# Kernel tuning notes

Measured on AMD Instinct MI355X. Metric: run time of the kernel, lower is better.

Reference implementation:

```python
import jax, jax.numpy as jnp
import numpy as np

ALPHA = 0.5
REG_RATIO = 0.5


def _xavier(key, shape):
    fan_in, fan_out = shape
    lim = np.sqrt(6.0 / (fan_in + fan_out))
    return jax.random.uniform(key, shape, minval=-lim, maxval=lim, dtype=jnp.float32)


def setup_inputs() -> dict:
    key = jax.random.key(0)
    ks = jax.random.split(key, 5)
    B, T, I, H, O = 128, 512, 4, 512, 3
    return {
        "x": jax.random.normal(ks[0], (B, T, I), dtype=jnp.float32),
        "h": jax.random.normal(ks[1], (B, H), dtype=jnp.float32),
        "W_rec": _xavier(ks[2], (H, H)),
        "W_in": _xavier(ks[3], (I, H)),
        "W_out": _xavier(ks[4], (H, O)),
        "bias_rec": jnp.zeros((H,), dtype=jnp.float32),
        "bias_in": jnp.zeros((H,), dtype=jnp.float32),
    }


def reference(x, h, W_rec, W_in, W_out, bias_rec, bias_in):
    # x: (B, T, I), h: (B, H)
    B, T, _ = x.shape
    H = h.shape[1]
    n_reg = round(H * REG_RATIO)
    alpha = jnp.asarray(ALPHA, x.dtype)
    # add_noise=False -> noise term is zero
    xt = jnp.swapaxes(x, 0, 1)                     # (T, B, I)
    flags = (jnp.arange(T) > 0).astype(x.dtype)    # z_old reg term skipped at t=0

    def step(carry, inp):
        h_prev, z_prev, reg = carry
        x_t, flag = inp
        # z = W_rec-recurrence + input drive (h_rec + h_in in the torch code)
        z_new = jnp.tanh(h_prev) @ W_rec + bias_rec + x_t @ W_in + bias_in  # (B, H)
        h_new = (1.0 - alpha) * h_prev + alpha * z_new
        # note: h_from_prev / (1 - alpha) == h_prev
        reg = (reg
               + jnp.sum((h_new[:, :n_reg] - h_prev[:, :n_reg]) ** 2)
               + flag * jnp.sum((z_new[:, :n_reg] - z_prev[:, :n_reg]) ** 2))
        out = h_new @ W_out                        # (B, O)
        return (h_new, z_new, reg), (h_new, out)

    init = (h, jnp.zeros_like(h), jnp.asarray(0.0, x.dtype))
    (_, _, reg), (hs, outs) = jax.lax.scan(step, init, (xt, flags))

    hidden_states = jnp.concatenate([h[None], hs], axis=0)  # (T+1, B, H)
    outputs = jnp.swapaxes(outs, 0, 1)                      # (B, T, O)
    tcr_reg = reg / T / B / n_reg
    return outputs, hidden_states, tcr_reg
```

## Files before the change

### kernel.cpp

```cpp
#include <hip/hip_runtime.h>
#include <math.h>


#define BB 128
#define TT 512
#define II 4
#define HH 512
#define OO 3
#define NREG_ 256

#define NTHREADS 512
#define MEMBERS 4
#define ROWS 2
#define NGROUPS 64
#define NBLOCKS (NGROUPS * MEMBERS)

typedef unsigned long long u64;
typedef unsigned int u32;
typedef __attribute__((ext_vector_type(2))) float f32x2;

__device__ __forceinline__ u64 aload(const u64* p) {
    return __hip_atomic_load(p, __ATOMIC_RELAXED, __HIP_MEMORY_SCOPE_AGENT);
}
__device__ __forceinline__ void astore(u64* p, u64 v) {
    __hip_atomic_store(p, v, __ATOMIC_RELAXED, __HIP_MEMORY_SCOPE_AGENT);
}
__device__ __forceinline__ float fast_tanh(float x) {
    float ax = fabsf(x);
    float e  = __expf(2.0f * ax);
    float r  = 1.0f - 2.0f * __builtin_amdgcn_rcpf(e + 1.0f);
    return copysignf(r, x);
}

#define R16(M) M(0) M(1) M(2) M(3) M(4) M(5) M(6) M(7) \
               M(8) M(9) M(10) M(11) M(12) M(13) M(14) M(15)

#define WLD(Q) \
    f32x2 w##Q##a, w##Q##b, w##Q##c, w##Q##d; \
    w##Q##a.x = Wp[(size_t)(4*Q+0)*HH]; w##Q##a.y = Wp[(size_t)(4*Q+0)*HH+64]; \
    w##Q##b.x = Wp[(size_t)(4*Q+1)*HH]; w##Q##b.y = Wp[(size_t)(4*Q+1)*HH+64]; \
    w##Q##c.x = Wp[(size_t)(4*Q+2)*HH]; w##Q##c.y = Wp[(size_t)(4*Q+2)*HH+64]; \
    w##Q##d.x = Wp[(size_t)(4*Q+3)*HH]; w##Q##d.y = Wp[(size_t)(4*Q+3)*HH+64];

#define KSTEP(K, W) { \
    u32 a0_ = __builtin_amdgcn_readlane(__float_as_uint(ar0), (K)); \
    u32 a1_ = __builtin_amdgcn_readlane(__float_as_uint(ar1), (K)); \
    u64 ab_ = (u64)a0_ | ((u64)a1_ << 32); \
    asm("v_pk_fma_f32 %0, %2, %3, %0 op_sel_hi:[1,0,1]\n\t" \
        "v_pk_fma_f32 %1, %2, %3, %1 op_sel:[0,1,0] op_sel_hi:[1,1,1]" \
        : "+v"(accA), "+v"(accB) : "s"(ab_), "v"(W)); }

#define MV(Q) KSTEP(4*Q+0, w##Q##a) KSTEP(4*Q+1, w##Q##b) \
              KSTEP(4*Q+2, w##Q##c) KSTEP(4*Q+3, w##Q##d)

__global__ __launch_bounds__(NTHREADS) __attribute__((amdgpu_waves_per_eu(2, 2)))
void rnn_main(const float* __restrict__ x,
              const float* __restrict__ h0,
              const float* __restrict__ W_rec,
              const float* __restrict__ W_in,
              const float* __restrict__ bias_rec,
              const float* __restrict__ bias_in,
              float* __restrict__ hidden,
              u64* __restrict__ abuf,
              float* __restrict__ partials)
{
    const int tid  = threadIdx.x;
    const int bid  = blockIdx.x;
    const int xcd  = bid & 7;
    const int onx  = bid >> 3;
    const int memb = onx & (MEMBERS - 1);
    const int group = xcd * 8 + (onx >> 2);
    const int r0   = group * ROWS;
    const int wid  = tid >> 6;
    const int lane = tid & 63;

    __shared__ float sc_s[2][ROWS][128][9];
    __shared__ float xbuf[ROWS * TT * II];
    __shared__ float win_s[II][128];
    __shared__ float ub_s[128];
    __shared__ float red_s[NTHREADS / 64];

    for (int idx = tid; idx < ROWS * TT * II; idx += NTHREADS) {
        int r = idx >> 11, rem = idx & (TT * II - 1);
        xbuf[idx] = x[(size_t)(r0 + r) * (TT * II) + rem];
    }
    if (tid < II * 128) {
        int i = tid >> 7, jj = tid & 127;
        win_s[i][jj] = W_in[i * HH + memb * 128 + jj];
    }
    if (tid < 128) {
        ub_s[tid] = bias_rec[memb * 128 + tid] + bias_in[memb * 128 + tid];
    }

    const float* Wp = W_rec + (size_t)(wid * 64) * HH + memb * 128 + lane;
    R16(WLD)

    const int fr  = tid >> 7;
    const int fj  = tid & 127;
    const int fjg = memb * 128 + fj;
    float hprev = 0.0f, zprev = 0.0f, racc = 0.0f;
    if (tid < ROWS * 128) {
        hprev = h0[(size_t)(r0 + fr) * HH + fjg];
        float a0v = fast_tanh(hprev);
        u64 pv = (u64)__float_as_uint(a0v) | ((u64)1u << 32);
        astore(&abuf[((size_t)(0 * BB + r0 + fr)) * HH + fjg], pv);
        hidden[(size_t)(r0 + fr) * HH + fjg] = hprev;
    }

#pragma unroll 1
    for (int t = 0; t < TT; ++t) {
        const int slot = t & 1;
        const u32 tagc = (u32)(t + 1);
        const u32 tagp = (u32)(t + 2);

        const u64* p0 = abuf + ((size_t)(slot * BB + r0)) * HH + wid * 64 + lane;
        const u64* p1 = p0 + HH;
        u64 u0, u1;
        for (;;) {
            u0 = aload(p0);
            u1 = aload(p1);
            bool ok = ((u32)(u0 >> 32) == tagc) & ((u32)(u1 >> 32) == tagc);
            if (__all(ok)) break;
        }
        float ar0 = __uint_as_float((u32)u0);
        float ar1 = __uint_as_float((u32)u1);

        f32x2 accA = {0.0f, 0.0f};
        f32x2 accB = {0.0f, 0.0f};
        R16(MV)

        sc_s[slot][0][lane][wid]      = accA.x;
        sc_s[slot][1][lane][wid]      = accA.y;
        sc_s[slot][0][lane + 64][wid] = accB.x;
        sc_s[slot][1][lane + 64][wid] = accB.y;
        __syncthreads();

        if (tid < ROWS * 128) {
            float q0 = sc_s[slot][fr][fj][0], q1 = sc_s[slot][fr][fj][1];
            float q2 = sc_s[slot][fr][fj][2], q3 = sc_s[slot][fr][fj][3];
            float q4 = sc_s[slot][fr][fj][4], q5 = sc_s[slot][fr][fj][5];
            float q6 = sc_s[slot][fr][fj][6], q7 = sc_s[slot][fr][fj][7];
            float z = ((q0 + q1) + (q2 + q3)) + ((q4 + q5) + (q6 + q7));
            z += ub_s[fj];
            const float* xr = &xbuf[fr * (TT * II) + t * II];
            z = fmaf(xr[0], win_s[0][fj], z);
            z = fmaf(xr[1], win_s[1][fj], z);
            z = fmaf(xr[2], win_s[2][fj], z);
            z = fmaf(xr[3], win_s[3][fj], z);
            float hn = 0.5f * hprev + 0.5f * z;
            float av = fast_tanh(hn);
            u64 pv = (u64)__float_as_uint(av) | ((u64)tagp << 32);
            astore(&abuf[((size_t)(((t + 1) & 1) * BB + r0 + fr)) * HH + fjg], pv);
            hidden[(size_t)(t + 1) * BB * HH + (size_t)(r0 + fr) * HH + fjg] = hn;
            if (fjg < NREG_) {
                float d1 = hn - hprev;
                racc = fmaf(d1, d1, racc);
                if (t > 0) { float d2 = z - zprev; racc = fmaf(d2, d2, racc); }
                zprev = z;
            }
            hprev = hn;
        }
    }

    for (int off = 32; off; off >>= 1) racc += __shfl_down(racc, off);
    if ((tid & 63) == 0) red_s[tid >> 6] = racc;
    __syncthreads();
    if (tid == 0) {
        float s = 0.0f;
        for (int i = 0; i < NTHREADS / 64; ++i) s += red_s[i];
        partials[bid] = s;
    }
}

__global__ __launch_bounds__(256)
void rnn_out(const float* __restrict__ hidden,
             const float* __restrict__ W_out,
             float* __restrict__ outputs)
{
    __shared__ float wout_s[HH * OO];
    const int tid = threadIdx.x;
    for (int i = tid; i < HH * OO; i += 256) wout_s[i] = W_out[i];
    __syncthreads();

    const int gid  = blockIdx.x * 4 + (tid >> 6);
    const int lane = tid & 63;
    const int b = gid >> 9;
    const int t = gid & (TT - 1);
    const float* hp = hidden + (size_t)(t + 1) * BB * HH + (size_t)b * HH;

    float o0 = 0.0f, o1 = 0.0f, o2 = 0.0f;
#pragma unroll
    for (int q = 0; q < 8; ++q) {
        int k = lane + 64 * q;
        float hv = hp[k];
        o0 = fmaf(hv, wout_s[k * 3 + 0], o0);
        o1 = fmaf(hv, wout_s[k * 3 + 1], o1);
        o2 = fmaf(hv, wout_s[k * 3 + 2], o2);
    }
    for (int off = 32; off; off >>= 1) {
        o0 += __shfl_down(o0, off);
        o1 += __shfl_down(o1, off);
        o2 += __shfl_down(o2, off);
    }
    if (lane == 0) {
        float* op = outputs + (size_t)(b * TT + t) * OO;
        op[0] = o0; op[1] = o1; op[2] = o2;
    }
}

__global__ __launch_bounds__(256)
void rnn_tcr(const float* __restrict__ partials, float* __restrict__ tcr)
{
    __shared__ float red[4];
    const int tid = threadIdx.x;
    float v = partials[tid];
    for (int off = 32; off; off >>= 1) v += __shfl_down(v, off);
    if ((tid & 63) == 0) red[tid >> 6] = v;
    __syncthreads();
    if (tid == 0) {
        float s = red[0] + red[1] + red[2] + red[3];
        *tcr = s * (1.0f / ((float)TT * (float)BB * (float)NREG_));
    }
}

extern "C" void kernel_launch(void* const* d_in, const int* in_sizes, int n_in,
                              void* d_out, int out_size, void* d_ws, size_t ws_size,
                              hipStream_t stream)
{
    (void)in_sizes; (void)n_in; (void)out_size; (void)ws_size;

    const float* x     = (const float*)d_in[0];
    const float* h0    = (const float*)d_in[1];
    const float* W_rec = (const float*)d_in[2];
    const float* W_in  = (const float*)d_in[3];
    const float* W_out = (const float*)d_in[4];
    const float* brec  = (const float*)d_in[5];
    const float* bin   = (const float*)d_in[6];

    float* out     = (float*)d_out;
    float* outputs = out;
    float* hidden  = out + (size_t)BB * TT * OO;
    float* tcr     = out + (size_t)BB * TT * OO + (size_t)(TT + 1) * BB * HH;

    u64* abuf = (u64*)d_ws;
    const size_t abuf_bytes = (size_t)2 * BB * HH * sizeof(u64);
    float* partials = (float*)((char*)d_ws + abuf_bytes);

    (void)hipMemsetAsync(d_ws, 0, abuf_bytes, stream);

    void* args[] = { (void*)&x, (void*)&h0, (void*)&W_rec, (void*)&W_in,
                     (void*)&brec, (void*)&bin, (void*)&hidden,
                     (void*)&abuf, (void*)&partials };
    (void)hipLaunchCooperativeKernel((const void*)rnn_main,
                                     dim3(NBLOCKS), dim3(NTHREADS),
                                     args, 0, stream);

    rnn_out<<<dim3((BB * TT) / 4), dim3(256), 0, stream>>>(hidden, W_out, outputs);
    rnn_tcr<<<dim3(1), dim3(256), 0, stream>>>(partials, tcr);
}
```

Before: 1.012 ms.

## Assign groups by runtime XCC ID and poll XCD-local L2 for handoff

Each block reads its hardware XCC ID and registers through atomic counters. The four members of a batch-row group are then placed on the same XCD whenever possible, instead of relying on the assumed round-robin mapping of blockIdx. Blocks in such groups also write their tagged activations to a second buffer with plain stores and poll it using sc0 loads, so the per-step exchange can be served from the shared XCD L2 rather than through agent-scope coherence. The agent-scope atomic buffer is still always written, and polling falls back to it after a bounded spin. The costs are a start-up rendezvous, a duplicate store every step, and reliance on L2-level visibility between blocks on one XCD.

Measured after the change: 2.168 ms. 114% more time.

```diff
diff --git a/kernel.cpp b/kernel.cpp
--- a/kernel.cpp
+++ b/kernel.cpp
@@ -14,6 +14,11 @@
 #define ROWS 2
 #define NGROUPS 64
 #define NBLOCKS (NGROUPS * MEMBERS)
+
+#define WS_ADAT  16384
+#define WS_FDAT  (WS_ADAT + 1048576)
+#define WS_PART  (WS_FDAT + 1048576)
+#define WS_ZERO  WS_PART
 
 typedef unsigned long long u64;
 typedef unsigned int u32;
@@ -61,24 +66,58 @@
               const float* __restrict__ bias_rec,
               const float* __restrict__ bias_in,
               float* __restrict__ hidden,
-              u64* __restrict__ abuf,
+              u32* __restrict__ ws_u32,
               float* __restrict__ partials)
 {
     const int tid  = threadIdx.x;
-    const int bid  = blockIdx.x;
-    const int xcd  = bid & 7;
-    const int onx  = bid >> 3;
-    const int memb = onx & (MEMBERS - 1);
-    const int group = xcd * 8 + (onx >> 2);
-    const int r0   = group * ROWS;
     const int wid  = tid >> 6;
     const int lane = tid & 63;
 
+    u64* adat = (u64*)((char*)ws_u32 + WS_ADAT);
+    u64* fdat = (u64*)((char*)ws_u32 + WS_FDAT);
+
+    __shared__ int sh_g, sh_mm, sh_fast;
     __shared__ float sc_s[2][ROWS][128][9];
     __shared__ float xbuf[ROWS * TT * II];
     __shared__ float win_s[II][128];
     __shared__ float ub_s[128];
     __shared__ float red_s[NTHREADS / 64];
+
+    if (tid == 0) {
+        u32 xcc;
+        asm volatile("s_getreg_b32 %0, hwreg(HW_REG_XCC_ID)" : "=s"(xcc));
+        int xcd = (int)(xcc & 7u);
+        u32* totalp = ws_u32;
+        u32* cnt    = ws_u32 + 1;
+        int rank = (int)atomicAdd(&cnt[xcd], 1u);
+        __hip_atomic_fetch_add(totalp, 1u, __ATOMIC_RELEASE, __HIP_MEMORY_SCOPE_AGENT);
+        while (__hip_atomic_load(totalp, __ATOMIC_ACQUIRE, __HIP_MEMORY_SCOPE_AGENT)
+               < (u32)NBLOCKS)
+            __builtin_amdgcn_s_sleep(2);
+        u32 c[8];
+        for (int i = 0; i < 8; ++i)
+            c[i] = __hip_atomic_load(&cnt[i], __ATOMIC_RELAXED, __HIP_MEMORY_SCOPE_AGENT);
+        int gb = 0, g = -1, mm = 0, fast = 0;
+        for (int xx = 0; xx < 8; ++xx) {
+            int ng = (int)(c[xx] >> 2);
+            if (xx == xcd && rank < 4 * ng) {
+                g = gb + (rank >> 2); mm = rank & 3; fast = 1;
+            }
+            gb += ng;
+        }
+        if (g < 0) {
+            int lidx = 0;
+            for (int xx = 0; xx < xcd; ++xx) lidx += (int)(c[xx] & 3u);
+            lidx += rank - 4 * (int)(c[xcd] >> 2);
+            g = gb + (lidx >> 2); mm = lidx & 3; fast = 0;
+        }
+        sh_g = g; sh_mm = mm; sh_fast = fast;
+    }
+    __syncthreads();
+    const int g    = sh_g;
+    const int memb = sh_mm;
+    const int fast = sh_fast;
+    const int r0   = g * ROWS;
 
     for (int idx = tid; idx < ROWS * TT * II; idx += NTHREADS) {
         int r = idx >> 11, rem = idx & (TT * II - 1);
@@ -103,27 +142,53 @@
         hprev = h0[(size_t)(r0 + fr) * HH + fjg];
         float a0v = fast_tanh(hprev);
         u64 pv = (u64)__float_as_uint(a0v) | ((u64)1u << 32);
-        astore(&abuf[((size_t)(0 * BB + r0 + fr)) * HH + fjg], pv);
+        size_t pidx = ((size_t)(0 * NGROUPS + g) * 2 + fr) * HH + fjg;
+        if (fast) fdat[pidx] = pv;
+        astore(&adat[pidx], pv);
         hidden[(size_t)(r0 + fr) * HH + fjg] = hprev;
     }
+
+    int fastmode = fast;
 
 #pragma unroll 1
     for (int t = 0; t < TT; ++t) {
         const int slot = t & 1;
         const u32 tagc = (u32)(t + 1);
-        const u32 tagp = (u32)(t + 2);
-
-        const u64* p0 = abuf + ((size_t)(slot * BB + r0)) * HH + wid * 64 + lane;
-        const u64* p1 = p0 + HH;
-        u64 u0, u1;
-        for (;;) {
-            u0 = aload(p0);
-            u1 = aload(p1);
-            bool ok = ((u32)(u0 >> 32) == tagc) & ((u32)(u1 >> 32) == tagc);
-            if (__all(ok)) break;
+
+        float ar0, ar1;
+        {
+            u64 u0 = 0, u1 = 0;
+            bool got = false;
+            const size_t base = ((size_t)(slot * NGROUPS + g) * 2) * HH
+                                + wid * 64 + lane;
+            if (fastmode) {
+                const u64* f0 = fdat + base;
+                const u64* f1 = f0 + HH;
+                int it = 0;
+                for (;;) {
+                    asm volatile("global_load_dwordx2 %0, %2, off sc0\n\t"
+                                 "global_load_dwordx2 %1, %3, off sc0\n\t"
+                                 "s_waitcnt vmcnt(0)"
+                                 : "=v"(u0), "=v"(u1)
+                                 : "v"(f0), "v"(f1) : "memory");
+                    bool ok = ((u32)(u0 >> 32) == tagc) & ((u32)(u1 >> 32) == tagc);
+                    if (__all(ok)) { got = true; break; }
+                    if (++it > 2048) { fastmode = 0; break; }
+                }
+            }
+            if (!got) {
+                const u64* p0 = adat + base;
+                const u64* p1 = p0 + HH;
+                for (;;) {
+                    u0 = aload(p0);
+                    u1 = aload(p1);
+                    bool ok = ((u32)(u0 >> 32) == tagc) & ((u32)(u1 >> 32) == tagc);
+                    if (__all(ok)) break;
+                }
+            }
+            ar0 = __uint_as_float((u32)u0);
+            ar1 = __uint_as_float((u32)u1);
         }
-        float ar0 = __uint_as_float((u32)u0);
-        float ar1 = __uint_as_float((u32)u1);
 
         f32x2 accA = {0.0f, 0.0f};
         f32x2 accB = {0.0f, 0.0f};
@@ -149,8 +214,11 @@
             z = fmaf(xr[3], win_s[3][fj], z);
             float hn = 0.5f * hprev + 0.5f * z;
             float av = fast_tanh(hn);
-            u64 pv = (u64)__float_as_uint(av) | ((u64)tagp << 32);
-            astore(&abuf[((size_t)(((t + 1) & 1) * BB + r0 + fr)) * HH + fjg], pv);
+            const int slot2 = (t + 1) & 1;
+            u64 pv = (u64)__float_as_uint(av) | ((u64)(tagc + 1) << 32);
+            size_t pidx = ((size_t)(slot2 * NGROUPS + g) * 2 + fr) * HH + fjg;
+            if (fast) fdat[pidx] = pv;
+            astore(&adat[pidx], pv);
             hidden[(size_t)(t + 1) * BB * HH + (size_t)(r0 + fr) * HH + fjg] = hn;
             if (fjg < NREG_) {
                 float d1 = hn - hprev;
@@ -168,7 +236,7 @@
     if (tid == 0) {
         float s = 0.0f;
         for (int i = 0; i < NTHREADS / 64; ++i) s += red_s[i];
-        partials[bid] = s;
+        partials[g * MEMBERS + memb] = s;
     }
 }
 
@@ -242,15 +310,14 @@
     float* hidden  = out + (size_t)BB * TT * OO;
     float* tcr     = out + (size_t)BB * TT * OO + (size_t)(TT + 1) * BB * HH;
 
-    u64* abuf = (u64*)d_ws;
-    const size_t abuf_bytes = (size_t)2 * BB * HH * sizeof(u64);
-    float* partials = (float*)((char*)d_ws + abuf_bytes);
-
-    (void)hipMemsetAsync(d_ws, 0, abuf_bytes, stream);
+    u32*   ws_u32   = (u32*)d_ws;
+    float* partials = (float*)((char*)d_ws + WS_PART);
+
+    (void)hipMemsetAsync(d_ws, 0, WS_ZERO, stream);
 
     void* args[] = { (void*)&x, (void*)&h0, (void*)&W_rec, (void*)&W_in,
                      (void*)&brec, (void*)&bin, (void*)&hidden,
-                     (void*)&abuf, (void*)&partials };
+                     (void*)&ws_u32, (void*)&partials };
     (void)hipLaunchCooperativeKernel((const void*)rnn_main,
                                      dim3(NBLOCKS), dim3(NTHREADS),
                                      args, 0, stream);
```
